# Kernel optimization log

Measured on AMD Instinct MI355X. Metric: run time of the kernel, lower is better.

The kernel has to match this reference:

```python
import jax, jax.numpy as jnp
import numpy as np

B, L, D, H = 4, 2048, 1024, 16
HD = D // H

def setup_inputs() -> dict:
    key = jax.random.key(0)
    ks = jax.random.split(key, 11)
    s = 1.0 / np.sqrt(D)
    return {
        "query": jax.random.normal(ks[0], (B, L, D), jnp.float32),
        "key": jax.random.normal(ks[1], (B, L, D), jnp.float32),
        "value": jax.random.normal(ks[2], (B, L, D), jnp.float32),
        "Wq": jax.random.normal(ks[3], (D, D), jnp.float32) * s,
        "bq": jnp.zeros((D,), jnp.float32),
        "Wk": jax.random.normal(ks[4], (D, D), jnp.float32) * s,
        "bk": jnp.zeros((D,), jnp.float32),
        "Wv": jax.random.normal(ks[5], (D, D), jnp.float32) * s,
        "bv": jnp.zeros((D,), jnp.float32),
        "Wo": jax.random.normal(ks[6], (D, D), jnp.float32) * s,
        "bo": jnp.zeros((D,), jnp.float32),
    }

def reference(query, key, value, Wq, bq, Wk, bk, Wv, bv, Wo, bo):
    b = query.shape[0]
    # linear projections (torch Linear: x @ W.T + b)
    Q = query @ Wq.T + bq
    K = key @ Wk.T + bk
    V = value @ Wv.T + bv
    # split heads -> [b, h, l, hd]
    Q = Q.reshape(b, -1, H, HD).transpose(0, 2, 1, 3)
    K = K.reshape(b, -1, H, HD).transpose(0, 2, 1, 3)
    V = V.reshape(b, -1, H, HD).transpose(0, 2, 1, 3)
    energy = jnp.einsum('bhqd,bhkd->bhqk', Q, K) / jnp.sqrt(jnp.float32(HD))
    attn = jax.nn.softmax(energy, axis=-1)
    x = jnp.einsum('bhqk,bhkd->bhqd', attn, V)
    x = x.transpose(0, 2, 1, 3).reshape(b, -1, D)
    return x @ Wo.T + bo
```

## Files before the change

### kernel.cpp

```cpp
#include <hip/hip_runtime.h>

typedef float floatx4 __attribute__((ext_vector_type(4)));
typedef short bf16x8 __attribute__((ext_vector_type(8)));
typedef const unsigned int __attribute__((address_space(1))) gas_u32;
typedef unsigned int __attribute__((address_space(3))) las_u32;

#if __has_builtin(__builtin_amdgcn_exp2f)
#define EXP2F(x) __builtin_amdgcn_exp2f(x)
#else
#define EXP2F(x) exp2f(x)
#endif

__device__ __forceinline__ unsigned short f2bf(float x) {
    unsigned int u = __float_as_uint(x);
    unsigned int r = u + 0x7fffu + ((u >> 16) & 1u);
    return (unsigned short)(r >> 16);
}

__device__ __forceinline__ unsigned int pack2bf_t(float lo, float hi) {
#if __has_builtin(__builtin_amdgcn_perm)
    return __builtin_amdgcn_perm(__float_as_uint(hi), __float_as_uint(lo), 0x07060302u);
#else
    return (__float_as_uint(lo) >> 16) | (__float_as_uint(hi) & 0xffff0000u);
#endif
}

__device__ __forceinline__ void g2l16(const void* g, void* l) {
    __builtin_amdgcn_global_load_lds((gas_u32*)(unsigned long long)g,
                                     (las_u32*)(unsigned int)(unsigned long long)l,
                                     16, 0, 0);
}

__global__ __launch_bounds__(256) void cvt7_kernel(
    const float* __restrict__ q, const float* __restrict__ k, const float* __restrict__ v,
    const float* __restrict__ wq, const float* __restrict__ wk, const float* __restrict__ wv,
    const float* __restrict__ wo,
    unsigned short* __restrict__ qb, unsigned short* __restrict__ kb,
    unsigned short* __restrict__ vb, unsigned short* __restrict__ wqb,
    unsigned short* __restrict__ wkb, unsigned short* __restrict__ wvb,
    unsigned short* __restrict__ wob) {
    const int ty = blockIdx.y;
    const float* src; unsigned short* dst; int n4;
    switch (ty) {
        case 0: src = q;  dst = qb;  n4 = 2097152; break;
        case 1: src = k;  dst = kb;  n4 = 2097152; break;
        case 2: src = v;  dst = vb;  n4 = 2097152; break;
        case 3: src = wq; dst = wqb; n4 = 262144;  break;
        case 4: src = wk; dst = wkb; n4 = 262144;  break;
        case 5: src = wv; dst = wvb; n4 = 262144;  break;
        default: src = wo; dst = wob; n4 = 262144; break;
    }
    int i = blockIdx.x * 256 + threadIdx.x;
    if (i >= n4) return;
    float4 x = ((const float4*)src)[i];
    ushort4 o;
    o.x = f2bf(x.x); o.y = f2bf(x.y); o.z = f2bf(x.z); o.w = f2bf(x.w);
    ((ushort4*)dst)[i] = o;
}

__global__ __launch_bounds__(256) void cvt1_kernel(const float* __restrict__ wo,
                                                   unsigned short* __restrict__ wob) {
    int i = blockIdx.x * 256 + threadIdx.x;
    float4 x = ((const float4*)wo)[i];
    ushort4 o;
    o.x = f2bf(x.x); o.y = f2bf(x.y); o.z = f2bf(x.z); o.w = f2bf(x.w);
    ((ushort4*)wob)[i] = o;
}

template <int OUT_MODE>
__device__ __forceinline__ void gemm256_body(const unsigned short* __restrict__ Asrc,
                                             const unsigned short* __restrict__ W,
                                             const float* __restrict__ bias,
                                             void* __restrict__ Cout,
                                             unsigned short* lds, int m0, int n0,
                                             float scale) {
    constexpr int K = 1024, N = 1024;
    const int t = threadIdx.x;
    const int lane = t & 63, w = t >> 6;
    const int lr = lane & 15, quad = lane >> 4;
    const int wrow = (w & 3) * 64, wcol = (w >> 2) * 64;

    const unsigned short* gA[4];
    const unsigned short* gB[2];
#pragma unroll
    for (int i = 0; i < 4; ++i) {
        int idx = t + 512 * i;
        int row = idx >> 3, sl = idx & 7;
        gA[i] = Asrc + (size_t)(m0 + row) * K + ((sl ^ (row & 7)) * 8);
    }
#pragma unroll
    for (int i = 0; i < 2; ++i) {
        int idx = t + 512 * i;
        int row = idx >> 3, sl = idx & 7;
        gB[i] = W + (size_t)(n0 + row) * K + ((sl ^ (row & 7)) * 8);
    }

    auto STAGE = [&](int buf, int kt) {
        unsigned short* dst = lds + buf * 24576;
#pragma unroll
        for (int i = 0; i < 4; ++i)
            g2l16(gA[i] + kt * 64, dst + (w * 64 + i * 512) * 8);
#pragma unroll
        for (int i = 0; i < 2; ++i)
            g2l16(gB[i] + kt * 64, dst + 16384 + (w * 64 + i * 512) * 8);
    };

    floatx4 acc[4][4];
#pragma unroll
    for (int i = 0; i < 4; ++i)
#pragma unroll
        for (int j = 0; j < 4; ++j) acc[i][j] = (floatx4){0.f, 0.f, 0.f, 0.f};

    const int sc0 = (quad ^ (lr & 7)) * 8;
    const int sc1 = sc0 ^ 32;

    auto COMPUTE = [&](int buf) {
        const unsigned short* Ab = lds + buf * 24576;
        const unsigned short* Bb = Ab + 16384;
#pragma unroll
        for (int kh = 0; kh < 2; ++kh) {
            const int sc = kh ? sc1 : sc0;
            bf16x8 af[4], bfr[4];
#pragma unroll
            for (int i = 0; i < 4; ++i)
                af[i] = *(const bf16x8*)&Ab[(wrow + i * 16 + lr) * 64 + sc];
#pragma unroll
            for (int j = 0; j < 4; ++j)
                bfr[j] = *(const bf16x8*)&Bb[(wcol + j * 16 + lr) * 64 + sc];
#pragma unroll
            for (int i = 0; i < 4; ++i)
#pragma unroll
                for (int j = 0; j < 4; ++j) {
                    if constexpr (OUT_MODE == 2)
                        acc[i][j] = __builtin_amdgcn_mfma_f32_16x16x32_bf16(bfr[j], af[i], acc[i][j], 0, 0, 0);
                    else
                        acc[i][j] = __builtin_amdgcn_mfma_f32_16x16x32_bf16(af[i], bfr[j], acc[i][j], 0, 0, 0);
                }
        }
    };

    STAGE(0, 0);
    STAGE(1, 1);
    for (int kt = 0; kt < 16; ++kt) {
        if (kt < 15) {
            asm volatile("s_waitcnt vmcnt(6)" ::: "memory");
        } else {
            asm volatile("s_waitcnt vmcnt(0)" ::: "memory");
        }
        __builtin_amdgcn_sched_barrier(0);
        __builtin_amdgcn_s_barrier();
        __builtin_amdgcn_sched_barrier(0);
        if (kt + 2 < 16) STAGE((kt + 2) % 3, kt + 2);
        __builtin_amdgcn_s_setprio(1);
        COMPUTE(kt % 3);
        __builtin_amdgcn_s_setprio(0);
    }

    if constexpr (OUT_MODE == 2) {
        const int b = m0 >> 11;
        unsigned short* VT = (unsigned short*)Cout;
#pragma unroll
        for (int i = 0; i < 4; ++i) {
#pragma unroll
            for (int j = 0; j < 4; ++j) {
#pragma unroll
                for (int r = 0; r < 4; ++r) {
                    int d = n0 + wcol + j * 16 + quad * 4 + r;
                    int tok = (m0 & 2047) + wrow + i * 16 + lr;
                    float val = acc[i][j][r] + bias[d];
                    int t6 = tok & 63;
                    int ntok = (tok & ~63) | ((((t6 >> 3) ^ (d & 7)) << 3)) | (t6 & 7);
                    VT[(((size_t)b * 16 + (d >> 6)) * 64 + (d & 63)) * 2048 + ntok] = f2bf(val);
                }
            }
        }
    } else if constexpr (OUT_MODE == 3) {
        unsigned short* C = (unsigned short*)Cout;
#pragma unroll
        for (int i = 0; i < 4; ++i) {
#pragma unroll
            for (int j = 0; j < 4; ++j) {
#pragma unroll
                for (int r = 0; r < 4; ++r) {
                    int row = m0 + wrow + i * 16 + quad * 4 + r;
                    int col = n0 + wcol + j * 16 + lr;
                    float val = acc[i][j][r] + bias[col];
                    int r6 = row & 63;
                    int srow = (r6 & 32) | (((r6 >> 2) & 1) << 4) |
                               (((r6 >> 3) & 3) << 2) | (r6 & 3);
                    int nrow = (row & ~63) | srow;
                    int c6 = col & 63;
                    int ncol = (col & ~63) | ((((c6 >> 3) ^ (srow & 7)) << 3)) | (c6 & 7);
                    C[(size_t)nrow * N + ncol] = f2bf(val);
                }
            }
        }
    } else if constexpr (OUT_MODE == 1) {
        unsigned short* C = (unsigned short*)Cout;
#pragma unroll
        for (int i = 0; i < 4; ++i) {
#pragma unroll
            for (int j = 0; j < 4; ++j) {
#pragma unroll
                for (int r = 0; r < 4; ++r) {
                    int row = m0 + wrow + i * 16 + quad * 4 + r;
                    int col = n0 + wcol + j * 16 + lr;
                    float val = (acc[i][j][r] + bias[col]) * scale;
                    C[(size_t)row * N + col] = f2bf(val);
                }
            }
        }
    } else {
#pragma unroll
        for (int i = 0; i < 4; ++i) {
#pragma unroll
            for (int j = 0; j < 4; ++j) {
#pragma unroll
                for (int r = 0; r < 4; ++r) {
                    int row = m0 + wrow + i * 16 + quad * 4 + r;
                    int col = n0 + wcol + j * 16 + lr;
                    ((float*)Cout)[(size_t)row * N + col] = acc[i][j][r] + bias[col];
                }
            }
        }
    }
}

__device__ __forceinline__ void gemm_swz256(int bx, int& m0, int& n0) {
    const int wid = (bx & 7) * 32 + (bx >> 3);
    m0 = (wid >> 3) * 256;
    n0 = (wid & 7) * 128;
}

__global__ __launch_bounds__(512) void gemm_qkv3(
    const unsigned short* __restrict__ qb, const unsigned short* __restrict__ wqb,
    const float* __restrict__ bq, unsigned short* __restrict__ Qp,
    const unsigned short* __restrict__ kb, const unsigned short* __restrict__ wkb,
    const float* __restrict__ bk, unsigned short* __restrict__ Kp,
    const unsigned short* __restrict__ vb, const unsigned short* __restrict__ wvb,
    const float* __restrict__ bv, unsigned short* __restrict__ VTp, float qscale) {
    __shared__ unsigned short lds[3 * 24576];
    int m0, n0;
    gemm_swz256(blockIdx.x, m0, n0);
    if (blockIdx.z == 0)
        gemm256_body<1>(qb, wqb, bq, Qp, lds, m0, n0, qscale);
    else if (blockIdx.z == 1)
        gemm256_body<3>(kb, wkb, bk, Kp, lds, m0, n0, 1.0f);
    else
        gemm256_body<2>(vb, wvb, bv, VTp, lds, m0, n0, 1.0f);
}

__global__ __launch_bounds__(512) void gemm_q(
    const unsigned short* __restrict__ qb, const unsigned short* __restrict__ wqb,
    const float* __restrict__ bq, unsigned short* __restrict__ Qp, float qscale) {
    __shared__ unsigned short lds[3 * 24576];
    int m0, n0;
    gemm_swz256(blockIdx.x, m0, n0);
    gemm256_body<1>(qb, wqb, bq, Qp, lds, m0, n0, qscale);
}

__global__ __launch_bounds__(512) void gemm_kv(
    const unsigned short* __restrict__ kb, const unsigned short* __restrict__ wkb,
    const float* __restrict__ bk, unsigned short* __restrict__ Kp,
    const unsigned short* __restrict__ vb, const unsigned short* __restrict__ wvb,
    const float* __restrict__ bv, unsigned short* __restrict__ VTp) {
    __shared__ unsigned short lds[3 * 24576];
    int m0, n0;
    gemm_swz256(blockIdx.x, m0, n0);
    if (blockIdx.z == 0)
        gemm256_body<3>(kb, wkb, bk, Kp, lds, m0, n0, 1.0f);
    else
        gemm256_body<2>(vb, wvb, bv, VTp, lds, m0, n0, 1.0f);
}

__global__ __launch_bounds__(512) void gemm_o(const unsigned short* __restrict__ A,
                                              const unsigned short* __restrict__ W,
                                              const float* __restrict__ bias,
                                              void* __restrict__ C) {
    __shared__ unsigned short lds[3 * 24576];
    int m0, n0;
    gemm_swz256(blockIdx.x, m0, n0);
    gemm256_body<0>(A, W, bias, C, lds, m0, n0, 1.0f);
}

__global__ __launch_bounds__(256, 2) void attn_kernel(const unsigned short* __restrict__ Qp,
                                                      const unsigned short* __restrict__ Kp,
                                                      const unsigned short* __restrict__ VTp,
                                                      unsigned short* __restrict__ Xp) {
    constexpr int L = 2048, D = 1024;
    __shared__ unsigned short Ks[2][64 * 64];
    __shared__ unsigned short Vt[2][64 * 64];

    const int t = threadIdx.x;
    const int hw = blockIdx.x + 8 * blockIdx.y + 128 * blockIdx.z;
    const int wid = (hw & 7) * 64 + (hw >> 3);
    const int q0 = (wid & 7) * 256;
    const int h = (wid >> 3) & 15;
    const int b = wid >> 7;
    const int lane = t & 63;
    const int w = t >> 6;
    const int lr = lane & 15;
    const int quad = lane >> 4;
    const int x7 = lr & 7;

    const size_t kbase = ((size_t)(b * L)) * D + (size_t)h * 64;
    const size_t vtbase = ((size_t)(b * 16 + h)) * 64 * 2048;

    auto stage_async = [&](int buf, int kb2) {
        int k0 = kb2 * 64;
#pragma unroll
        for (int i = 0; i < 2; ++i) {
            int idx = t + 256 * i;
            int row = idx >> 3, c16 = idx & 7;
            g2l16(Kp + kbase + (size_t)(k0 + row) * D + c16 * 8,
                  &Ks[buf][(w * 64 + i * 256) * 8]);
            g2l16(VTp + vtbase + (size_t)row * 2048 + k0 + c16 * 8,
                  &Vt[buf][(w * 64 + i * 256) * 8]);
        }
    };

    stage_async(0, 0);

    const size_t qbase = ((size_t)(b * L + q0)) * D + (size_t)h * 64;
    bf16x8 bq[4][2];
#pragma unroll
    for (int qs = 0; qs < 4; ++qs)
#pragma unroll
        for (int s2 = 0; s2 < 2; ++s2)
            bq[qs][s2] = *(const bf16x8*)(Qp + qbase + (size_t)(w * 64 + qs * 16 + lr) * D +
                                          s2 * 32 + quad * 8);

    floatx4 o[4][4], ol[4];
#pragma unroll
    for (int qs = 0; qs < 4; ++qs) {
        ol[qs] = (floatx4){0.f, 0.f, 0.f, 0.f};
#pragma unroll
        for (int dt = 0; dt < 4; ++dt) o[qs][dt] = (floatx4){0.f, 0.f, 0.f, 0.f};
    }
    bf16x8 ones;
#pragma unroll
    for (int e = 0; e < 8; ++e) ones[e] = (short)0x3F80;

    __syncthreads();
    int cur = 0;

    const int kc0 = (quad ^ x7) * 8;
    const int kc1 = ((quad + 4) ^ x7) * 8;

    for (int kb = 0; kb < L / 64; ++kb) {
        if (kb < L / 64 - 1) stage_async(cur ^ 1, kb + 1);

        __builtin_amdgcn_s_setprio(1);
#pragma unroll
        for (int g = 0; g < 2; ++g) {
            bf16x8 akA0 = *(const bf16x8*)&Ks[cur][(g * 32 + lr) * 64 + kc0];
            bf16x8 akA1 = *(const bf16x8*)&Ks[cur][(g * 32 + lr) * 64 + kc1];
            bf16x8 akB0 = *(const bf16x8*)&Ks[cur][(g * 32 + 16 + lr) * 64 + kc0];
            bf16x8 akB1 = *(const bf16x8*)&Ks[cur][(g * 32 + 16 + lr) * 64 + kc1];
            bf16x8 vf[4];
#pragma unroll
            for (int dt = 0; dt < 4; ++dt)
                vf[dt] = *(const bf16x8*)&Vt[cur][(dt * 16 + lr) * 64 +
                                                  (((g * 4 + quad) ^ x7) * 8)];

            const floatx4 z4 = (floatx4){0.f, 0.f, 0.f, 0.f};
#pragma unroll
            for (int qs = 0; qs < 4; ++qs) {
                floatx4 stA = __builtin_amdgcn_mfma_f32_16x16x32_bf16(akA0, bq[qs][0], z4, 0, 0, 0);
                stA = __builtin_amdgcn_mfma_f32_16x16x32_bf16(akA1, bq[qs][1], stA, 0, 0, 0);
                floatx4 stB = __builtin_amdgcn_mfma_f32_16x16x32_bf16(akB0, bq[qs][0], z4, 0, 0, 0);
                stB = __builtin_amdgcn_mfma_f32_16x16x32_bf16(akB1, bq[qs][1], stB, 0, 0, 0);

                union { unsigned int u[4]; bf16x8 v; } pf;
                pf.u[0] = pack2bf_t(EXP2F(stA[0]), EXP2F(stA[1]));
                pf.u[1] = pack2bf_t(EXP2F(stA[2]), EXP2F(stA[3]));
                pf.u[2] = pack2bf_t(EXP2F(stB[0]), EXP2F(stB[1]));
                pf.u[3] = pack2bf_t(EXP2F(stB[2]), EXP2F(stB[3]));

                ol[qs] = __builtin_amdgcn_mfma_f32_16x16x32_bf16(pf.v, ones, ol[qs], 0, 0, 0);
#pragma unroll
                for (int dt = 0; dt < 4; ++dt)
                    o[qs][dt] = __builtin_amdgcn_mfma_f32_16x16x32_bf16(pf.v, vf[dt],
                                                                        o[qs][dt], 0, 0, 0);
            }
        }
        __builtin_amdgcn_s_setprio(0);

        if (kb < L / 64 - 1) {
            __syncthreads();
            cur ^= 1;
        }
    }

#pragma unroll
    for (int qs = 0; qs < 4; ++qs) {
#pragma unroll
        for (int r = 0; r < 4; ++r) {
            float inv = 1.0f / ol[qs][r];
            int q = q0 + w * 64 + qs * 16 + quad * 4 + r;
            size_t base = ((size_t)(b * L + q)) * D + (size_t)h * 64;
#pragma unroll
            for (int dt = 0; dt < 4; ++dt)
                Xp[base + dt * 16 + lr] = f2bf(o[qs][dt][r] * inv);
        }
    }
}

extern "C" void kernel_launch(void* const* d_in, const int* in_sizes, int n_in,
                              void* d_out, int out_size, void* d_ws, size_t ws_size,
                              hipStream_t stream) {
    const float* query = (const float*)d_in[0];
    const float* key_  = (const float*)d_in[1];
    const float* value = (const float*)d_in[2];
    const float* Wq = (const float*)d_in[3];
    const float* bq = (const float*)d_in[4];
    const float* Wk = (const float*)d_in[5];
    const float* bk = (const float*)d_in[6];
    const float* Wv = (const float*)d_in[7];
    const float* bv = (const float*)d_in[8];
    const float* Wo = (const float*)d_in[9];
    const float* bo = (const float*)d_in[10];
    float* out = (float*)d_out;

    const size_t MB16 = (size_t)8 * 1024 * 1024;

    unsigned short* Qp  = (unsigned short*)d_ws;
    unsigned short* kb  = Qp + MB16;
    unsigned short* vb  = kb + MB16;
    unsigned short* VTp = vb + MB16;
    unsigned short* Xp  = kb;
    unsigned short* Kp  = (unsigned short*)d_out;
    unsigned short* wqb = Kp + MB16;
    unsigned short* wkb = wqb + 1024 * 1024;
    unsigned short* wvb = wkb + 1024 * 1024;

    const float qscale = 0.125f * 1.44269504f;
    dim3 bb(256);

    const bool bigws = ws_size >= (size_t)82 * 1024 * 1024;

    if (bigws) {
        unsigned short* qb  = VTp + MB16;
        unsigned short* wob = qb + MB16;
        cvt7_kernel<<<dim3(8192, 7), bb, 0, stream>>>(query, key_, value, Wq, Wk, Wv, Wo,
                                                      qb, kb, vb, wqb, wkb, wvb, wob);
        gemm_qkv3<<<dim3(256, 1, 3), dim3(512), 0, stream>>>(qb, wqb, bq, Qp,
                                                             kb, wkb, bk, Kp,
                                                             vb, wvb, bv, VTp, qscale);
        attn_kernel<<<dim3(8, 16, 4), bb, 0, stream>>>(Qp, Kp, VTp, Xp);
        gemm_o<<<dim3(256), dim3(512), 0, stream>>>(Xp, wob, bo, out);
    } else {
        unsigned short* qb  = (unsigned short*)d_out;
        unsigned short* wob = vb;
        cvt7_kernel<<<dim3(8192, 6), bb, 0, stream>>>(query, key_, value, Wq, Wk, Wv, Wo,
                                                      qb, kb, vb, wqb, wkb, wvb, nullptr);
        gemm_q<<<dim3(256), dim3(512), 0, stream>>>(qb, wqb, bq, Qp, qscale);
        gemm_kv<<<dim3(256, 1, 2), dim3(512), 0, stream>>>(kb, wkb, bk, Kp,
                                                           vb, wvb, bv, VTp);
        attn_kernel<<<dim3(8, 16, 4), bb, 0, stream>>>(Qp, Kp, VTp, Xp);
        cvt1_kernel<<<dim3(1024), bb, 0, stream>>>(Wo, wob);
        gemm_o<<<dim3(256), dim3(512), 0, stream>>>(Xp, wob, bo, out);
    }
}
```

Before: 303.6 us.

## Halve GEMM K-tile to shrink LDS and raise occupancy; flatten conversion grid

The GEMM K-step drops from 64 to 32, so the triple-buffered LDS footprint halves and the swizzle is adjusted for 32-element rows. Launch bounds now request 4 blocks per CU of 512 threads, aiming for more resident waves to hide latency. In exchange the loop runs twice as many iterations with a barrier each, and the register cap from the launch bound may cause spills. The conversion kernel also moves to a 1D grid with no idle blocks, instead of a 2D grid where the weight rows left most blocks exiting early.

```diff
diff --git a/kernel.cpp b/kernel.cpp
--- a/kernel.cpp
+++ b/kernel.cpp
@@ -31,7 +31,7 @@
                                      16, 0, 0);
 }
 
-__global__ __launch_bounds__(256) void cvt7_kernel(
+__global__ __launch_bounds__(256) void cvt_kernel(
     const float* __restrict__ q, const float* __restrict__ k, const float* __restrict__ v,
     const float* __restrict__ wq, const float* __restrict__ wk, const float* __restrict__ wv,
     const float* __restrict__ wo,
@@ -39,23 +39,26 @@
     unsigned short* __restrict__ vb, unsigned short* __restrict__ wqb,
     unsigned short* __restrict__ wkb, unsigned short* __restrict__ wvb,
     unsigned short* __restrict__ wob) {
-    const int ty = blockIdx.y;
-    const float* src; unsigned short* dst; int n4;
-    switch (ty) {
-        case 0: src = q;  dst = qb;  n4 = 2097152; break;
-        case 1: src = k;  dst = kb;  n4 = 2097152; break;
-        case 2: src = v;  dst = vb;  n4 = 2097152; break;
-        case 3: src = wq; dst = wqb; n4 = 262144;  break;
-        case 4: src = wk; dst = wkb; n4 = 262144;  break;
-        case 5: src = wv; dst = wvb; n4 = 262144;  break;
-        default: src = wo; dst = wob; n4 = 262144; break;
-    }
-    int i = blockIdx.x * 256 + threadIdx.x;
-    if (i >= n4) return;
-    float4 x = ((const float4*)src)[i];
+    const int bid = blockIdx.x;
+    const float* src;
+    unsigned short* dst;
+    int off;
+    if (bid < 24576) {
+        int s = bid >> 13;
+        off = (bid & 8191) * 256 + threadIdx.x;
+        src = (s == 0) ? q : (s == 1) ? k : v;
+        dst = (s == 0) ? qb : (s == 1) ? kb : vb;
+    } else {
+        int r = bid - 24576;
+        int s = r >> 10;
+        off = (r & 1023) * 256 + threadIdx.x;
+        src = (s == 0) ? wq : (s == 1) ? wk : (s == 2) ? wv : wo;
+        dst = (s == 0) ? wqb : (s == 1) ? wkb : (s == 2) ? wvb : wob;
+    }
+    float4 x = ((const float4*)src)[off];
     ushort4 o;
     o.x = f2bf(x.x); o.y = f2bf(x.y); o.z = f2bf(x.z); o.w = f2bf(x.w);
-    ((ushort4*)dst)[i] = o;
+    ((ushort4*)dst)[off] = o;
 }
 
 __global__ __launch_bounds__(256) void cvt1_kernel(const float* __restrict__ wo,
@@ -75,82 +78,75 @@
                                              unsigned short* lds, int m0, int n0,
                                              float scale) {
     constexpr int K = 1024, N = 1024;
+    constexpr int ABUF = 256 * 32;
+    constexpr int BUFS = ABUF + 128 * 32;
     const int t = threadIdx.x;
     const int lane = t & 63, w = t >> 6;
     const int lr = lane & 15, quad = lane >> 4;
     const int wrow = (w & 3) * 64, wcol = (w >> 2) * 64;
 
-    const unsigned short* gA[4];
-    const unsigned short* gB[2];
-#pragma unroll
-    for (int i = 0; i < 4; ++i) {
-        int idx = t + 512 * i;
-        int row = idx >> 3, sl = idx & 7;
-        gA[i] = Asrc + (size_t)(m0 + row) * K + ((sl ^ (row & 7)) * 8);
-    }
+    const unsigned short* gA[2];
+    const unsigned short* gB;
 #pragma unroll
     for (int i = 0; i < 2; ++i) {
         int idx = t + 512 * i;
-        int row = idx >> 3, sl = idx & 7;
-        gB[i] = W + (size_t)(n0 + row) * K + ((sl ^ (row & 7)) * 8);
+        int row = idx >> 2, sl = idx & 3;
+        gA[i] = Asrc + (size_t)(m0 + row) * K + ((sl ^ ((row >> 1) & 3)) * 8);
+    }
+    {
+        int row = t >> 2, sl = t & 3;
+        gB = W + (size_t)(n0 + row) * K + ((sl ^ ((row >> 1) & 3)) * 8);
     }
 
     auto STAGE = [&](int buf, int kt) {
-        unsigned short* dst = lds + buf * 24576;
+        unsigned short* dst = lds + buf * BUFS;
+#pragma unroll
+        for (int i = 0; i < 2; ++i)
+            g2l16(gA[i] + kt * 32, dst + (w * 64 + i * 512) * 8);
+        g2l16(gB + kt * 32, dst + ABUF + (w * 64) * 8);
+    };
+
+    floatx4 acc[4][4];
+#pragma unroll
+    for (int i = 0; i < 4; ++i)
+#pragma unroll
+        for (int j = 0; j < 4; ++j) acc[i][j] = (floatx4){0.f, 0.f, 0.f, 0.f};
+
+    const int sc = (quad ^ ((lr >> 1) & 3)) * 8;
+
+    auto COMPUTE = [&](int buf) {
+        const unsigned short* Ab = lds + buf * BUFS;
+        const unsigned short* Bb = Ab + ABUF;
+        bf16x8 af[4], bfr[4];
 #pragma unroll
         for (int i = 0; i < 4; ++i)
-            g2l16(gA[i] + kt * 64, dst + (w * 64 + i * 512) * 8);
-#pragma unroll
-        for (int i = 0; i < 2; ++i)
-            g2l16(gB[i] + kt * 64, dst + 16384 + (w * 64 + i * 512) * 8);
-    };
-
-    floatx4 acc[4][4];
-#pragma unroll
-    for (int i = 0; i < 4; ++i)
-#pragma unroll
-        for (int j = 0; j < 4; ++j) acc[i][j] = (floatx4){0.f, 0.f, 0.f, 0.f};
-
-    const int sc0 = (quad ^ (lr & 7)) * 8;
-    const int sc1 = sc0 ^ 32;
-
-    auto COMPUTE = [&](int buf) {
-        const unsigned short* Ab = lds + buf * 24576;
-        const unsigned short* Bb = Ab + 16384;
-#pragma unroll
-        for (int kh = 0; kh < 2; ++kh) {
-            const int sc = kh ? sc1 : sc0;
-            bf16x8 af[4], bfr[4];
-#pragma unroll
-            for (int i = 0; i < 4; ++i)
-                af[i] = *(const bf16x8*)&Ab[(wrow + i * 16 + lr) * 64 + sc];
-#pragma unroll
-            for (int j = 0; j < 4; ++j)
-                bfr[j] = *(const bf16x8*)&Bb[(wcol + j * 16 + lr) * 64 + sc];
-#pragma unroll
-            for (int i = 0; i < 4; ++i)
-#pragma unroll
-                for (int j = 0; j < 4; ++j) {
-                    if constexpr (OUT_MODE == 2)
-                        acc[i][j] = __builtin_amdgcn_mfma_f32_16x16x32_bf16(bfr[j], af[i], acc[i][j], 0, 0, 0);
-                    else
-                        acc[i][j] = __builtin_amdgcn_mfma_f32_16x16x32_bf16(af[i], bfr[j], acc[i][j], 0, 0, 0);
-                }
-        }
+            af[i] = *(const bf16x8*)&Ab[(wrow + i * 16 + lr) * 32 + sc];
+#pragma unroll
+        for (int j = 0; j < 4; ++j)
+            bfr[j] = *(const bf16x8*)&Bb[(wcol + j * 16 + lr) * 32 + sc];
+#pragma unroll
+        for (int i = 0; i < 4; ++i)
+#pragma unroll
+            for (int j = 0; j < 4; ++j) {
+                if constexpr (OUT_MODE == 2)
+                    acc[i][j] = __builtin_amdgcn_mfma_f32_16x16x32_bf16(bfr[j], af[i], acc[i][j], 0, 0, 0);
+                else
+                    acc[i][j] = __builtin_amdgcn_mfma_f32_16x16x32_bf16(af[i], bfr[j], acc[i][j], 0, 0, 0);
+            }
     };
 
     STAGE(0, 0);
     STAGE(1, 1);
-    for (int kt = 0; kt < 16; ++kt) {
-        if (kt < 15) {
-            asm volatile("s_waitcnt vmcnt(6)" ::: "memory");
+    for (int kt = 0; kt < 32; ++kt) {
+        if (kt < 31) {
+            asm volatile("s_waitcnt vmcnt(3)" ::: "memory");
         } else {
             asm volatile("s_waitcnt vmcnt(0)" ::: "memory");
         }
         __builtin_amdgcn_sched_barrier(0);
         __builtin_amdgcn_s_barrier();
         __builtin_amdgcn_sched_barrier(0);
-        if (kt + 2 < 16) STAGE((kt + 2) % 3, kt + 2);
+        if (kt + 2 < 32) STAGE((kt + 2) % 3, kt + 2);
         __builtin_amdgcn_s_setprio(1);
         COMPUTE(kt % 3);
         __builtin_amdgcn_s_setprio(0);
@@ -232,14 +228,14 @@
     n0 = (wid & 7) * 128;
 }
 
-__global__ __launch_bounds__(512) void gemm_qkv3(
+__global__ __launch_bounds__(512, 4) void gemm_qkv3(
     const unsigned short* __restrict__ qb, const unsigned short* __restrict__ wqb,
     const float* __restrict__ bq, unsigned short* __restrict__ Qp,
     const unsigned short* __restrict__ kb, const unsigned short* __restrict__ wkb,
     const float* __restrict__ bk, unsigned short* __restrict__ Kp,
     const unsigned short* __restrict__ vb, const unsigned short* __restrict__ wvb,
     const float* __restrict__ bv, unsigned short* __restrict__ VTp, float qscale) {
-    __shared__ unsigned short lds[3 * 24576];
+    __shared__ unsigned short lds[3 * 12288];
     int m0, n0;
     gemm_swz256(blockIdx.x, m0, n0);
     if (blockIdx.z == 0)
@@ -250,21 +246,21 @@
         gemm256_body<2>(vb, wvb, bv, VTp, lds, m0, n0, 1.0f);
 }
 
-__global__ __launch_bounds__(512) void gemm_q(
+__global__ __launch_bounds__(512, 4) void gemm_q(
     const unsigned short* __restrict__ qb, const unsigned short* __restrict__ wqb,
     const float* __restrict__ bq, unsigned short* __restrict__ Qp, float qscale) {
-    __shared__ unsigned short lds[3 * 24576];
+    __shared__ unsigned short lds[3 * 12288];
     int m0, n0;
     gemm_swz256(blockIdx.x, m0, n0);
     gemm256_body<1>(qb, wqb, bq, Qp, lds, m0, n0, qscale);
 }
 
-__global__ __launch_bounds__(512) void gemm_kv(
+__global__ __launch_bounds__(512, 4) void gemm_kv(
     const unsigned short* __restrict__ kb, const unsigned short* __restrict__ wkb,
     const float* __restrict__ bk, unsigned short* __restrict__ Kp,
     const unsigned short* __restrict__ vb, const unsigned short* __restrict__ wvb,
     const float* __restrict__ bv, unsigned short* __restrict__ VTp) {
-    __shared__ unsigned short lds[3 * 24576];
+    __shared__ unsigned short lds[3 * 12288];
     int m0, n0;
     gemm_swz256(blockIdx.x, m0, n0);
     if (blockIdx.z == 0)
@@ -273,11 +269,11 @@
         gemm256_body<2>(vb, wvb, bv, VTp, lds, m0, n0, 1.0f);
 }
 
-__global__ __launch_bounds__(512) void gemm_o(const unsigned short* __restrict__ A,
-                                              const unsigned short* __restrict__ W,
-                                              const float* __restrict__ bias,
-                                              void* __restrict__ C) {
-    __shared__ unsigned short lds[3 * 24576];
+__global__ __launch_bounds__(512, 4) void gemm_o(const unsigned short* __restrict__ A,
+                                                 const unsigned short* __restrict__ W,
+                                                 const float* __restrict__ bias,
+                                                 void* __restrict__ C) {
+    __shared__ unsigned short lds[3 * 12288];
     int m0, n0;
     gemm_swz256(blockIdx.x, m0, n0);
     gemm256_body<0>(A, W, bias, C, lds, m0, n0, 1.0f);
@@ -442,8 +438,8 @@
     if (bigws) {
         unsigned short* qb  = VTp + MB16;
         unsigned short* wob = qb + MB16;
-        cvt7_kernel<<<dim3(8192, 7), bb, 0, stream>>>(query, key_, value, Wq, Wk, Wv, Wo,
-                                                      qb, kb, vb, wqb, wkb, wvb, wob);
+        cvt_kernel<<<dim3(24576 + 4096), bb, 0, stream>>>(query, key_, value, Wq, Wk, Wv, Wo,
+                                                          qb, kb, vb, wqb, wkb, wvb, wob);
         gemm_qkv3<<<dim3(256, 1, 3), dim3(512), 0, stream>>>(qb, wqb, bq, Qp,
                                                              kb, wkb, bk, Kp,
                                                              vb, wvb, bv, VTp, qscale);
@@ -452,8 +448,8 @@
     } else {
         unsigned short* qb  = (unsigned short*)d_out;
         unsigned short* wob = vb;
-        cvt7_kernel<<<dim3(8192, 6), bb, 0, stream>>>(query, key_, value, Wq, Wk, Wv, Wo,
-                                                      qb, kb, vb, wqb, wkb, wvb, nullptr);
+        cvt_kernel<<<dim3(24576 + 3072), bb, 0, stream>>>(query, key_, value, Wq, Wk, Wv, Wo,
+                                                          qb, kb, vb, wqb, wkb, wvb, nullptr);
         gemm_q<<<dim3(256), dim3(512), 0, stream>>>(qb, wqb, bq, Qp, qscale);
         gemm_kv<<<dim3(256, 1, 2), dim3(512), 0, stream>>>(kb, wkb, bk, Kp,
                                                            vb, wvb, bv, VTp);
```

New measurement: 298.8 us (median of 2 runs). No clear change (-1.6%).
